# Kernel optimization log

Hardware: AMD Instinct MI355X
Metric: run time of the kernel (lower is better)

The kernel has to match this reference:

```python
import jax, jax.numpy as jnp
import numpy as np

DIM = 512
N_HEADS = 8
HEAD_DIM = DIM // N_HEADS
BN_EPS = 1e-5


def setup_inputs() -> dict:
    key = jax.random.key(0)
    ks = jax.random.split(key, 8)
    B, C, H, W = 16, DIM, 32, 32
    x = jax.random.normal(ks[0], (B, C, H, W), dtype=jnp.float32)
    # 1x1 convs == channel matmuls: stacked q/k/v weights [3, out, in], proj [out, in]
    w_qkv = jax.random.normal(ks[1], (3, DIM, DIM), dtype=jnp.float32) * (DIM ** -0.5)
    w_proj = jax.random.normal(ks[2], (DIM, DIM), dtype=jnp.float32) * (DIM ** -0.5)
    # BatchNorm (inference form) params for q/k/v branches, stacked [3, C]
    bn_gamma = jax.random.uniform(ks[3], (3, DIM), minval=0.5, maxval=1.5)
    bn_beta = jax.random.normal(ks[4], (3, DIM)) * 0.1
    bn_mean = jax.random.normal(ks[5], (3, DIM)) * 0.1
    bn_var = jax.random.uniform(ks[6], (3, DIM), minval=0.5, maxval=1.5)
    return {"x": x, "w_qkv": w_qkv, "w_proj": w_proj, "bn_gamma": bn_gamma,
            "bn_beta": bn_beta, "bn_mean": bn_mean, "bn_var": bn_var}


def _ternary_ste(t):
    # forward: sign(t) in {-1,0,1}; backward: identity (straight-through)
    return t + jax.lax.stop_gradient(jnp.sign(t) - t)


def reference(x, w_qkv, w_proj, bn_gamma, bn_beta, bn_mean, bn_var):
    B, C, H, W = x.shape
    N = H * W
    xf = x.reshape(B, C, N)
    # fused 1x1 conv for q,k,v: [3,B,C,N]
    qkv = jnp.einsum('koc,bcn->kbon', w_qkv, xf)
    # BatchNorm (inference): y = (x - mean)/sqrt(var+eps)*gamma + beta
    s = bn_gamma / jnp.sqrt(bn_var + BN_EPS)          # [3,C]
    b = bn_beta - bn_mean * s                          # [3,C]
    qkv = qkv * s[:, None, :, None] + b[:, None, :, None]
    q = _ternary_ste(qkv[0]).reshape(B, N_HEADS, HEAD_DIM, N)
    k = _ternary_ste(qkv[1]).reshape(B, N_HEADS, HEAD_DIM, N)
    v = qkv[2].reshape(B, N_HEADS, HEAD_DIM, N)
    scale = HEAD_DIM ** -0.5
    attn = jnp.einsum('bhdn,bhen->bhde', q, k) * scale  # [B,h,d,d] channel-wise attn
    attn = jax.nn.softmax(attn, axis=-1)
    out = jnp.einsum('bhde,bhen->bhdn', attn, v).reshape(B, C, N)
    out = jnp.einsum('oc,bcn->bon', w_proj, out) + xf   # proj + residual
    return out.reshape(B, C, H, W)
```

## Files before the change

kernel.cpp:

```cpp
#include <hip/hip_runtime.h>
#include <math.h>

#define BN_EPS 1e-5f

typedef _Float16 f16;
typedef _Float16 f16x4 __attribute__((ext_vector_type(4)));
typedef _Float16 f16x8 __attribute__((ext_vector_type(8)));
typedef float f32x4 __attribute__((ext_vector_type(4)));
typedef int i32x4 __attribute__((ext_vector_type(4)));

static constexpr int BB = 16;
static constexpr int C  = 512;
static constexpr int NP = 1024;
static constexpr int NH = 8;
static constexpr int HD = 64;
static constexpr int M3 = 1536;

static constexpr size_t OFF_WHI = 0;
static constexpr size_t OFF_WLO = 1572864;
static constexpr size_t OFF_WPH = 3145728;
static constexpr size_t OFF_SB  = 3670016;
static constexpr size_t OFF_XTH = 3682304;
static constexpr size_t OFF_XTL = 20459520;
static constexpr size_t OFF_AOT = OFF_XTH;
static constexpr size_t OFF_Q   = 37236736;
static constexpr size_t OFF_K   = 45625344;
static constexpr size_t OFF_VT  = 54013952;

__device__ __forceinline__ void gld16(const void* g, void* l) {
  __builtin_amdgcn_global_load_lds(
      (const __attribute__((address_space(1))) void*)g,
      (__attribute__((address_space(3))) void*)l, 16, 0, 0);
}

__global__ __launch_bounds__(256) void k_convW(
    const float* __restrict__ wqkv, const float* __restrict__ wproj,
    const float* __restrict__ g, const float* __restrict__ be,
    const float* __restrict__ mu, const float* __restrict__ va,
    f16* __restrict__ Whi, f16* __restrict__ Wlo, f16* __restrict__ Wph,
    float* __restrict__ sA, float* __restrict__ bA)
{
  const int i = blockIdx.x * 256 + threadIdx.x;
  if (i < M3 * C) {
    const float w = wqkv[i];
    const f16 h = (f16)w;
    Whi[i] = h;
    Wlo[i] = (f16)(w - (float)h);
  }
  if (i < C * C) Wph[i] = (f16)wproj[i];
  if (i < M3) {
    const float s = g[i] / sqrtf(va[i] + BN_EPS);
    sA[i] = s;
    bA[i] = be[i] - mu[i] * s;
  }
}

__global__ __launch_bounds__(256) void k_convX(
    const float* __restrict__ x, f16* __restrict__ XtH, f16* __restrict__ XtL)
{
  const int k0 = blockIdx.x * 64, n0 = blockIdx.y * 64, b = blockIdx.z;
  __shared__ float ls[64][65];
  const int t = threadIdx.x;
  const float* xp = x + ((size_t)b * C + k0) * NP + n0;
  const int c4 = (t & 15) * 4, r0 = t >> 4;
#pragma unroll
  for (int q = 0; q < 4; ++q) {
    const float4 v = *(const float4*)(xp + (size_t)(r0 + q * 16) * NP + c4);
    ls[r0 + q * 16][c4 + 0] = v.x; ls[r0 + q * 16][c4 + 1] = v.y;
    ls[r0 + q * 16][c4 + 2] = v.z; ls[r0 + q * 16][c4 + 3] = v.w;
  }
  __syncthreads();
  const int n = t >> 2, kk = (t & 3) * 16;
  f16x8 hv0 = {}, hv1 = {}, lv0 = {}, lv1 = {};
#pragma unroll
  for (int q = 0; q < 8; ++q) {
    float v = ls[kk + q][n];
    f16 h = (f16)v;
    hv0[q] = h; lv0[q] = (f16)(v - (float)h);
  }
#pragma unroll
  for (int q = 0; q < 8; ++q) {
    float v = ls[kk + 8 + q][n];
    f16 h = (f16)v;
    hv1[q] = h; lv1[q] = (f16)(v - (float)h);
  }
  const size_t o = ((size_t)b * NP + n0 + n) * C + k0 + kk;
  *(f16x8*)&XtH[o] = hv0; *(f16x8*)&XtH[o + 8] = hv1;
  *(f16x8*)&XtL[o] = lv0; *(f16x8*)&XtL[o + 8] = lv1;
}

__global__ __launch_bounds__(256) void k_qkv_mfma(
    const f16* __restrict__ Whi, const f16* __restrict__ Wlo,
    const f16* __restrict__ XtH, const f16* __restrict__ XtL,
    const float* __restrict__ sA, const float* __restrict__ bA,
    signed char* __restrict__ qw, signed char* __restrict__ kw,
    f16* __restrict__ vt)
{
  __shared__ __align__(16) f16 SMEM[4 * 128 * 32];
  f16* Ah = SMEM;
  f16* Al = SMEM + 4096;
  f16* Bh = SMEM + 8192;
  f16* Bl = SMEM + 12288;

  const int t = threadIdx.x, lane = t & 63, wid = t >> 6;
  const int n0 = blockIdx.x * 128, m0 = blockIdx.y * 128, b = blockIdx.z;

  const f16* A0h = Whi + (size_t)m0 * C;
  const f16* A0l = Wlo + (size_t)m0 * C;
  const f16* B0h = XtH + ((size_t)b * NP + n0) * C;
  const f16* B0l = XtL + ((size_t)b * NP + n0) * C;

  f32x4 acc[4][4];
#pragma unroll
  for (int i = 0; i < 4; ++i)
#pragma unroll
    for (int j = 0; j < 4; ++j) acc[i][j] = (f32x4){0.f, 0.f, 0.f, 0.f};

  const int wm = wid >> 1, wn = wid & 1;
  const int lr = lane & 15, ls = lane >> 4;
  const int srow = wid * 16 + (lane >> 2);
  const int scol = (lane & 3) * 8;

  for (int kc = 0; kc < 512; kc += 32) {
#pragma unroll
    for (int r = 0; r < 2; ++r) {
      const size_t go = (size_t)(r * 64 + srow) * C + kc + scol;
      const int lo = (r * 64 + wid * 16) * 32;
      gld16(A0h + go, &Ah[lo]);
      gld16(A0l + go, &Al[lo]);
      gld16(B0h + go, &Bh[lo]);
      gld16(B0l + go, &Bl[lo]);
    }
    __syncthreads();

    f16x8 ah[4], al[4], bh[4], bl[4];
#pragma unroll
    for (int i = 0; i < 4; ++i) {
      const int ao = (wm * 64 + i * 16 + lr) * 32 + ls * 8;
      ah[i] = *(const f16x8*)&Ah[ao];
      al[i] = *(const f16x8*)&Al[ao];
      const int bo = (wn * 64 + i * 16 + lr) * 32 + ls * 8;
      bh[i] = *(const f16x8*)&Bh[bo];
      bl[i] = *(const f16x8*)&Bl[bo];
    }
#pragma unroll
    for (int i = 0; i < 4; ++i)
#pragma unroll
      for (int j = 0; j < 4; ++j) {
        acc[i][j] = __builtin_amdgcn_mfma_f32_16x16x32_f16(ah[i], bh[j], acc[i][j], 0, 0, 0);
        acc[i][j] = __builtin_amdgcn_mfma_f32_16x16x32_f16(ah[i], bl[j], acc[i][j], 0, 0, 0);
        acc[i][j] = __builtin_amdgcn_mfma_f32_16x16x32_f16(al[i], bh[j], acc[i][j], 0, 0, 0);
      }
    __syncthreads();
  }

  const int kidx = m0 >> 9;
  if (kidx != 2) {
    signed char* dst0 = (kidx == 0) ? qw : kw;
#pragma unroll
    for (int i = 0; i < 4; ++i) {
      float sv[4], bv[4];
#pragma unroll
      for (int r = 0; r < 4; ++r) {
        const int o = m0 + wm * 64 + i * 16 + ls * 4 + r;
        sv[r] = sA[o]; bv[r] = bA[o];
      }
      const int oc0 = (m0 & 511) + wm * 64 + i * 16 + ls * 4;
#pragma unroll
      for (int j = 0; j < 4; ++j) {
        const int n = n0 + wn * 64 + j * 16 + lr;
#pragma unroll
        for (int r = 0; r < 4; ++r) {
          const float y = fmaf(acc[i][j][r], sv[r], bv[r]);
          dst0[((size_t)b * C + oc0 + r) * NP + n] =
              (signed char)((y > 0.f) - (y < 0.f));
        }
      }
    }
  } else {
    const int c0 = m0 & 511;
    for (int hf = 0; hf < 2; ++hf) {
      __syncthreads();
      if (wn == hf) {
#pragma unroll
        for (int i = 0; i < 4; ++i) {
          float sv[4], bv[4];
#pragma unroll
          for (int r = 0; r < 4; ++r) {
            const int o = m0 + wm * 64 + i * 16 + ls * 4 + r;
            sv[r] = sA[o]; bv[r] = bA[o];
          }
#pragma unroll
          for (int j = 0; j < 4; ++j) {
            f16x4 pk;
#pragma unroll
            for (int r = 0; r < 4; ++r)
              pk[r] = (f16)fmaf(acc[i][j][r], sv[r], bv[r]);
            *(f16x4*)&SMEM[(size_t)(j * 16 + lr) * 136 + wm * 64 + i * 16 + ls * 4] = pk;
          }
        }
      }
      __syncthreads();
      const int nl = t >> 2, cc = (t & 3) * 32;
      const f16* src = &SMEM[(size_t)nl * 136 + cc];
      f16x8 r0 = *(const f16x8*)(src + 0);
      f16x8 r1 = *(const f16x8*)(src + 8);
      f16x8 r2 = *(const f16x8*)(src + 16);
      f16x8 r3 = *(const f16x8*)(src + 24);
      f16* dstv = vt + ((size_t)b * NP + n0 + hf * 64 + nl) * C + c0 + cc;
      *(f16x8*)(dstv + 0)  = r0;
      *(f16x8*)(dstv + 8)  = r1;
      *(f16x8*)(dstv + 16) = r2;
      *(f16x8*)(dstv + 24) = r3;
    }
  }
}

__global__ __launch_bounds__(256) void k_attn_fused(
    const signed char* __restrict__ qw, const signed char* __restrict__ kw,
    const f16* __restrict__ vt, f16* __restrict__ aot)
{
  const int half = blockIdx.x;
  const int bh = blockIdx.y;
  const int b = bh >> 3, h = bh & 7;
  const int t = threadIdx.x, lane = t & 63, wid = t >> 6;
  const int dw = wid * 16;
  const int lr = lane & 15, lg = lane >> 4;

  __shared__ f16 ph[64][72];
  __shared__ f16 pl[64][72];
  __shared__ f16 sb[64][72];

  const signed char* qp = qw + ((size_t)b * C + h * HD + dw + lr) * NP;
  const signed char* kp = kw + ((size_t)b * C + h * HD + lr) * NP;

  i32x4 accS[4];
#pragma unroll
  for (int j = 0; j < 4; ++j) accS[j] = (i32x4){0, 0, 0, 0};

#pragma unroll 4
  for (int ks = 0; ks < 16; ++ks) {
    const i32x4 af = *(const i32x4*)(qp + ks * 64 + lg * 16);
#pragma unroll
    for (int j = 0; j < 4; ++j) {
      const i32x4 bf = *(const i32x4*)(kp + (size_t)(j * 16) * NP + ks * 64 + lg * 16);
      accS[j] = __builtin_amdgcn_mfma_i32_16x16x64_i8(af, bf, accS[j], 0, 0, 0);
    }
  }

#pragma unroll
  for (int r = 0; r < 4; ++r) {
    float mx = (float)accS[0][r];
#pragma unroll
    for (int j = 1; j < 4; ++j) mx = fmaxf(mx, (float)accS[j][r]);
    mx = fmaxf(mx, __shfl_xor(mx, 1));
    mx = fmaxf(mx, __shfl_xor(mx, 2));
    mx = fmaxf(mx, __shfl_xor(mx, 4));
    mx = fmaxf(mx, __shfl_xor(mx, 8));
    float pvv[4];
    float sm = 0.f;
#pragma unroll
    for (int j = 0; j < 4; ++j) {
      pvv[j] = expf(((float)accS[j][r] - mx) * 0.125f);
      sm += pvv[j];
    }
    sm += __shfl_xor(sm, 1);
    sm += __shfl_xor(sm, 2);
    sm += __shfl_xor(sm, 4);
    sm += __shfl_xor(sm, 8);
    const float inv = 1.f / sm;
    const int drow = dw + lg * 4 + r;
#pragma unroll
    for (int j = 0; j < 4; ++j) {
      const float p = pvv[j] * inv;
      const f16 hi = (f16)p;
      ph[drow][j * 16 + lr] = hi;
      pl[drow][j * 16 + lr] = (f16)(p - (float)hi);
    }
  }
  __syncthreads();

  const f16x8 pa0h = *(const f16x8*)&ph[dw + lr][lg * 8];
  const f16x8 pa0l = *(const f16x8*)&pl[dw + lr][lg * 8];
  const f16x8 pa1h = *(const f16x8*)&ph[dw + lr][32 + lg * 8];
  const f16x8 pa1l = *(const f16x8*)&pl[dw + lr][32 + lg * 8];

  const f16* vbase = vt + (size_t)b * NP * C + h * HD;
  const int nbase = half * 512;

  for (int nc = 0; nc < 8; ++nc) {
    const int nn0 = nbase + nc * 64;
    __syncthreads();
#pragma unroll
    for (int nt = 0; nt < 4; ++nt) {
      const f16* vp = vbase + (size_t)(nn0 + nt * 16 + lr) * C + lg * 8;
      const f16x8 bv0 = *(const f16x8*)(vp);
      const f16x8 bv1 = *(const f16x8*)(vp + 32);
      f32x4 acc = (f32x4){0.f, 0.f, 0.f, 0.f};
      acc = __builtin_amdgcn_mfma_f32_16x16x32_f16(pa0h, bv0, acc, 0, 0, 0);
      acc = __builtin_amdgcn_mfma_f32_16x16x32_f16(pa0l, bv0, acc, 0, 0, 0);
      acc = __builtin_amdgcn_mfma_f32_16x16x32_f16(pa1h, bv1, acc, 0, 0, 0);
      acc = __builtin_amdgcn_mfma_f32_16x16x32_f16(pa1l, bv1, acc, 0, 0, 0);
      f16x4 pk;
#pragma unroll
      for (int r = 0; r < 4; ++r) pk[r] = (f16)acc[r];
      *(f16x4*)&sb[nt * 16 + lr][dw + lg * 4] = pk;
    }
    __syncthreads();
    const int nl = t >> 2, cc = (t & 3) * 16;
    const f16x8 o0 = *(const f16x8*)&sb[nl][cc];
    const f16x8 o1 = *(const f16x8*)&sb[nl][cc + 8];
    f16* dst = aot + ((size_t)b * NP + nn0 + nl) * C + h * HD + cc;
    *(f16x8*)(dst + 0) = o0;
    *(f16x8*)(dst + 8) = o1;
  }
}

__global__ __launch_bounds__(256) void k_proj_mfma(
    const f16* __restrict__ Wph, const f16* __restrict__ aot,
    const float* __restrict__ X, float* __restrict__ out)
{
  __shared__ __align__(16) f16 Ah[128 * 32];
  __shared__ __align__(16) f16 Bh[128 * 32];

  const int t = threadIdx.x, lane = t & 63, wid = t >> 6;
  const int n0 = blockIdx.x * 128, m0 = blockIdx.y * 128, b = blockIdx.z;

  const f16* A0 = Wph + (size_t)m0 * C;
  const f16* B0 = aot + ((size_t)b * NP + n0) * C;

  f32x4 acc[4][4];
#pragma unroll
  for (int i = 0; i < 4; ++i)
#pragma unroll
    for (int j = 0; j < 4; ++j) acc[i][j] = (f32x4){0.f, 0.f, 0.f, 0.f};

  const int wm = wid >> 1, wn = wid & 1;
  const int lr = lane & 15, ls = lane >> 4;
  const int srow = wid * 16 + (lane >> 2);
  const int scol = (lane & 3) * 8;

  for (int kc = 0; kc < 512; kc += 32) {
#pragma unroll
    for (int r = 0; r < 2; ++r) {
      const size_t go = (size_t)(r * 64 + srow) * C + kc + scol;
      const int lo = (r * 64 + wid * 16) * 32;
      gld16(A0 + go, &Ah[lo]);
      gld16(B0 + go, &Bh[lo]);
    }
    __syncthreads();

    f16x8 ah[4], bh[4];
#pragma unroll
    for (int i = 0; i < 4; ++i) {
      ah[i] = *(const f16x8*)&Ah[(wm * 64 + i * 16 + lr) * 32 + ls * 8];
      bh[i] = *(const f16x8*)&Bh[(wn * 64 + i * 16 + lr) * 32 + ls * 8];
    }
#pragma unroll
    for (int i = 0; i < 4; ++i)
#pragma unroll
      for (int j = 0; j < 4; ++j)
        acc[i][j] = __builtin_amdgcn_mfma_f32_16x16x32_f16(ah[i], bh[j], acc[i][j], 0, 0, 0);
    __syncthreads();
  }

#pragma unroll
  for (int i = 0; i < 4; ++i) {
    const int oc0 = m0 + wm * 64 + i * 16 + ls * 4;
#pragma unroll
    for (int j = 0; j < 4; ++j) {
      const int n = n0 + wn * 64 + j * 16 + lr;
#pragma unroll
      for (int r = 0; r < 4; ++r) {
        const size_t idx = ((size_t)b * C + oc0 + r) * NP + n;
        out[idx] = acc[i][j][r] + X[idx];
      }
    }
  }
}

extern "C" void kernel_launch(void* const* d_in, const int* in_sizes, int n_in,
                              void* d_out, int out_size, void* d_ws, size_t ws_size,
                              hipStream_t stream)
{
  const float* x      = (const float*)d_in[0];
  const float* w_qkv  = (const float*)d_in[1];
  const float* w_proj = (const float*)d_in[2];
  const float* g      = (const float*)d_in[3];
  const float* be     = (const float*)d_in[4];
  const float* mu     = (const float*)d_in[5];
  const float* va     = (const float*)d_in[6];
  float* out = (float*)d_out;

  char* ws = (char*)d_ws;
  f16*  Whi = (f16*)(ws + OFF_WHI);
  f16*  Wlo = (f16*)(ws + OFF_WLO);
  f16*  Wph = (f16*)(ws + OFF_WPH);
  float* sA = (float*)(ws + OFF_SB);
  float* bA = sA + M3;
  f16*  XtH = (f16*)(ws + OFF_XTH);
  f16*  XtL = (f16*)(ws + OFF_XTL);
  f16*  aot = (f16*)(ws + OFF_AOT);
  signed char* qw = (signed char*)(ws + OFF_Q);
  signed char* kw = (signed char*)(ws + OFF_K);
  f16*  vtw = (f16*)(ws + OFF_VT);

  k_convW<<<dim3((M3 * C + 255) / 256), 256, 0, stream>>>(
      w_qkv, w_proj, g, be, mu, va, Whi, Wlo, Wph, sA, bA);
  k_convX<<<dim3(C / 64, NP / 64, BB), 256, 0, stream>>>(x, XtH, XtL);
  k_qkv_mfma<<<dim3(NP / 128, M3 / 128, BB), 256, 0, stream>>>(
      Whi, Wlo, XtH, XtL, sA, bA, qw, kw, vtw);
  k_attn_fused<<<dim3(2, BB * NH), 256, 0, stream>>>(qw, kw, vtw, aot);
  k_proj_mfma<<<dim3(NP / 128, C / 128, BB), 256, 0, stream>>>(Wph, aot, x, out);
}
```

Measured before the change: 152.2 us.

## Use single f16 MFMA for QKV with flagged split-precision sign fixup

Replaces the three-MFMA hi/lo split-precision QKV GEMM with a single f16 MFMA. It computes per-row weight norms and per-pixel input norms so that q/k outputs whose magnitude falls within an error bound of zero can be flagged in a bitmask. A new fixup kernel recomputes only the flagged sign values with hi+lo precision dot products. This cuts the main GEMM's MFMA work and shared-memory traffic by about two thirds, at the cost of extra memsets, atomics, a norm kernel and a sparse fixup pass. The heuristic bound constant, and V now using only the f16 high part, carry accuracy risk.

```diff
diff --git a/kernel.cpp b/kernel.cpp
--- a/kernel.cpp
+++ b/kernel.cpp
@@ -2,6 +2,7 @@
 #include <math.h>
 
 #define BN_EPS 1e-5f
+#define FIXC 3.0e-4f
 
 typedef _Float16 f16;
 typedef _Float16 f16x4 __attribute__((ext_vector_type(4)));
@@ -16,16 +17,19 @@
 static constexpr int HD = 64;
 static constexpr int M3 = 1536;
 
-static constexpr size_t OFF_WHI = 0;
-static constexpr size_t OFF_WLO = 1572864;
-static constexpr size_t OFF_WPH = 3145728;
-static constexpr size_t OFF_SB  = 3670016;
-static constexpr size_t OFF_XTH = 3682304;
-static constexpr size_t OFF_XTL = 20459520;
-static constexpr size_t OFF_AOT = OFF_XTH;
-static constexpr size_t OFF_Q   = 37236736;
-static constexpr size_t OFF_K   = 45625344;
-static constexpr size_t OFF_VT  = 54013952;
+static constexpr size_t OFF_WHI  = 0;
+static constexpr size_t OFF_WLO  = 1572864;
+static constexpr size_t OFF_WPH  = 3145728;
+static constexpr size_t OFF_SB   = 3670016;
+static constexpr size_t OFF_WN   = 3682304;
+static constexpr size_t OFF_XN   = 3686400;
+static constexpr size_t OFF_FLAG = 3751936;
+static constexpr size_t OFF_XTH  = 5849088;
+static constexpr size_t OFF_XTL  = 22626304;
+static constexpr size_t OFF_AOT  = OFF_XTH;
+static constexpr size_t OFF_Q    = 39403520;
+static constexpr size_t OFF_K    = 47792128;
+static constexpr size_t OFF_VT   = 56180736;
 
 __device__ __forceinline__ void gld16(const void* g, void* l) {
   __builtin_amdgcn_global_load_lds(
@@ -55,8 +59,23 @@
   }
 }
 
+__global__ __launch_bounds__(256) void k_wnorm(
+    const float* __restrict__ wqkv, float* __restrict__ wnorm)
+{
+  const int row = blockIdx.x * 4 + (threadIdx.x >> 6);
+  const int lane = threadIdx.x & 63;
+  const float4 v0 = *(const float4*)&wqkv[(size_t)row * C + lane * 8];
+  const float4 v1 = *(const float4*)&wqkv[(size_t)row * C + lane * 8 + 4];
+  float s = v0.x * v0.x + v0.y * v0.y + v0.z * v0.z + v0.w * v0.w
+          + v1.x * v1.x + v1.y * v1.y + v1.z * v1.z + v1.w * v1.w;
+  s += __shfl_xor(s, 1);  s += __shfl_xor(s, 2);  s += __shfl_xor(s, 4);
+  s += __shfl_xor(s, 8);  s += __shfl_xor(s, 16); s += __shfl_xor(s, 32);
+  if (lane == 0) wnorm[row] = sqrtf(s);
+}
+
 __global__ __launch_bounds__(256) void k_convX(
-    const float* __restrict__ x, f16* __restrict__ XtH, f16* __restrict__ XtL)
+    const float* __restrict__ x, f16* __restrict__ XtH, f16* __restrict__ XtL,
+    float* __restrict__ xnorm2)
 {
   const int k0 = blockIdx.x * 64, n0 = blockIdx.y * 64, b = blockIdx.z;
   __shared__ float ls[64][65];
@@ -70,6 +89,12 @@
     ls[r0 + q * 16][c4 + 2] = v.z; ls[r0 + q * 16][c4 + 3] = v.w;
   }
   __syncthreads();
+  if (t < 64) {
+    float s2 = 0.f;
+#pragma unroll
+    for (int q = 0; q < 64; ++q) { const float v = ls[q][t]; s2 = fmaf(v, v, s2); }
+    atomicAdd(&xnorm2[(b << 10) + n0 + t], s2);
+  }
   const int n = t >> 2, kk = (t & 3) * 16;
   f16x8 hv0 = {}, hv1 = {}, lv0 = {}, lv1 = {};
 #pragma unroll
@@ -90,25 +115,21 @@
 }
 
 __global__ __launch_bounds__(256) void k_qkv_mfma(
-    const f16* __restrict__ Whi, const f16* __restrict__ Wlo,
-    const f16* __restrict__ XtH, const f16* __restrict__ XtL,
+    const f16* __restrict__ Whi, const f16* __restrict__ XtH,
     const float* __restrict__ sA, const float* __restrict__ bA,
+    const float* __restrict__ wnorm, const float* __restrict__ xnorm2,
     signed char* __restrict__ qw, signed char* __restrict__ kw,
-    f16* __restrict__ vt)
-{
-  __shared__ __align__(16) f16 SMEM[4 * 128 * 32];
+    f16* __restrict__ vt, unsigned* __restrict__ flagbits)
+{
+  __shared__ __align__(16) f16 SMEM[8704];
   f16* Ah = SMEM;
-  f16* Al = SMEM + 4096;
-  f16* Bh = SMEM + 8192;
-  f16* Bl = SMEM + 12288;
+  f16* Bh = SMEM + 4096;
 
   const int t = threadIdx.x, lane = t & 63, wid = t >> 6;
   const int n0 = blockIdx.x * 128, m0 = blockIdx.y * 128, b = blockIdx.z;
 
   const f16* A0h = Whi + (size_t)m0 * C;
-  const f16* A0l = Wlo + (size_t)m0 * C;
   const f16* B0h = XtH + ((size_t)b * NP + n0) * C;
-  const f16* B0l = XtL + ((size_t)b * NP + n0) * C;
 
   f32x4 acc[4][4];
 #pragma unroll
@@ -127,53 +148,54 @@
       const size_t go = (size_t)(r * 64 + srow) * C + kc + scol;
       const int lo = (r * 64 + wid * 16) * 32;
       gld16(A0h + go, &Ah[lo]);
-      gld16(A0l + go, &Al[lo]);
       gld16(B0h + go, &Bh[lo]);
-      gld16(B0l + go, &Bl[lo]);
-    }
-    __syncthreads();
-
-    f16x8 ah[4], al[4], bh[4], bl[4];
+    }
+    __syncthreads();
+    f16x8 ah[4], bh[4];
 #pragma unroll
     for (int i = 0; i < 4; ++i) {
-      const int ao = (wm * 64 + i * 16 + lr) * 32 + ls * 8;
-      ah[i] = *(const f16x8*)&Ah[ao];
-      al[i] = *(const f16x8*)&Al[ao];
-      const int bo = (wn * 64 + i * 16 + lr) * 32 + ls * 8;
-      bh[i] = *(const f16x8*)&Bh[bo];
-      bl[i] = *(const f16x8*)&Bl[bo];
+      ah[i] = *(const f16x8*)&Ah[(wm * 64 + i * 16 + lr) * 32 + ls * 8];
+      bh[i] = *(const f16x8*)&Bh[(wn * 64 + i * 16 + lr) * 32 + ls * 8];
     }
 #pragma unroll
     for (int i = 0; i < 4; ++i)
 #pragma unroll
-      for (int j = 0; j < 4; ++j) {
+      for (int j = 0; j < 4; ++j)
         acc[i][j] = __builtin_amdgcn_mfma_f32_16x16x32_f16(ah[i], bh[j], acc[i][j], 0, 0, 0);
-        acc[i][j] = __builtin_amdgcn_mfma_f32_16x16x32_f16(ah[i], bl[j], acc[i][j], 0, 0, 0);
-        acc[i][j] = __builtin_amdgcn_mfma_f32_16x16x32_f16(al[i], bh[j], acc[i][j], 0, 0, 0);
-      }
     __syncthreads();
   }
 
   const int kidx = m0 >> 9;
   if (kidx != 2) {
     signed char* dst0 = (kidx == 0) ? qw : kw;
+    float xnrm[4];
+#pragma unroll
+    for (int j = 0; j < 4; ++j)
+      xnrm[j] = sqrtf(xnorm2[(b << 10) + n0 + wn * 64 + j * 16 + lr]);
 #pragma unroll
     for (int i = 0; i < 4; ++i) {
-      float sv[4], bv[4];
+      float sv[4], bv[4], dl[4];
 #pragma unroll
       for (int r = 0; r < 4; ++r) {
         const int o = m0 + wm * 64 + i * 16 + ls * 4 + r;
         sv[r] = sA[o]; bv[r] = bA[o];
+        dl[r] = FIXC * wnorm[o] * sv[r];
       }
       const int oc0 = (m0 & 511) + wm * 64 + i * 16 + ls * 4;
+      const int og0 = m0 + wm * 64 + i * 16 + ls * 4;
 #pragma unroll
       for (int j = 0; j < 4; ++j) {
         const int n = n0 + wn * 64 + j * 16 + lr;
 #pragma unroll
         for (int r = 0; r < 4; ++r) {
-          const float y = fmaf(acc[i][j][r], sv[r], bv[r]);
+          const float z = fmaf(acc[i][j][r], sv[r], bv[r]);
           dst0[((size_t)b * C + oc0 + r) * NP + n] =
-              (signed char)((y > 0.f) - (y < 0.f));
+              (signed char)((z > 0.f) - (z < 0.f));
+          if (fabsf(z) <= dl[r] * xnrm[j]) {
+            const int of = og0 + r;
+            atomicOr(&flagbits[(((size_t)b * NP + n) << 5) + (of >> 5)],
+                     1u << (of & 31));
+          }
         }
       }
     }
@@ -216,6 +238,51 @@
   }
 }
 
+__global__ __launch_bounds__(256) void k_fix(
+    const unsigned* __restrict__ flagbits,
+    const f16* __restrict__ Whi, const f16* __restrict__ Wlo,
+    const f16* __restrict__ XtH, const f16* __restrict__ XtL,
+    const float* __restrict__ sA, const float* __restrict__ bA,
+    signed char* __restrict__ qw, signed char* __restrict__ kw)
+{
+  const int wv = blockIdx.x * 4 + (threadIdx.x >> 6);
+  const int lane = threadIdx.x & 63;
+  const int b = wv >> 10, n = wv & 1023;
+
+  const unsigned* bm = flagbits + ((size_t)wv << 5);
+  const unsigned myw = (lane < 32) ? bm[lane] : 0u;
+  if (__ballot(myw != 0) == 0ULL) return;
+
+  const size_t xo = ((size_t)b * NP + n) * C + lane * 8;
+  const f16x8 bhv = *(const f16x8*)&XtH[xo];
+  const f16x8 blv = *(const f16x8*)&XtL[xo];
+  float xv[8];
+#pragma unroll
+  for (int q = 0; q < 8; ++q) xv[q] = (float)bhv[q] + (float)blv[q];
+
+  for (int w = 0; w < 32; ++w) {
+    unsigned bits = __shfl(myw, w);
+    while (bits) {
+      const int o = w * 32 + __builtin_ctz(bits);
+      bits &= bits - 1;
+      const f16x8 ahv = *(const f16x8*)&Whi[(size_t)o * C + lane * 8];
+      const f16x8 alv = *(const f16x8*)&Wlo[(size_t)o * C + lane * 8];
+      float s = 0.f;
+#pragma unroll
+      for (int q = 0; q < 8; ++q)
+        s = fmaf((float)ahv[q] + (float)alv[q], xv[q], s);
+      s += __shfl_xor(s, 1);  s += __shfl_xor(s, 2);  s += __shfl_xor(s, 4);
+      s += __shfl_xor(s, 8);  s += __shfl_xor(s, 16); s += __shfl_xor(s, 32);
+      if (lane == 0) {
+        const float y = fmaf(s, sA[o], bA[o]);
+        const signed char sg = (signed char)((y > 0.f) - (y < 0.f));
+        if (o < 512) qw[((size_t)b * C + o) * NP + n] = sg;
+        else         kw[((size_t)b * C + (o - 512)) * NP + n] = sg;
+      }
+    }
+  }
+}
+
 __global__ __launch_bounds__(256) void k_attn_fused(
     const signed char* __restrict__ qw, const signed char* __restrict__ kw,
     const f16* __restrict__ vt, f16* __restrict__ aot)
@@ -398,6 +465,9 @@
   f16*  Wph = (f16*)(ws + OFF_WPH);
   float* sA = (float*)(ws + OFF_SB);
   float* bA = sA + M3;
+  float* wn = (float*)(ws + OFF_WN);
+  float* xn2 = (float*)(ws + OFF_XN);
+  unsigned* flagbits = (unsigned*)(ws + OFF_FLAG);
   f16*  XtH = (f16*)(ws + OFF_XTH);
   f16*  XtL = (f16*)(ws + OFF_XTL);
   f16*  aot = (f16*)(ws + OFF_AOT);
@@ -405,11 +475,17 @@
   signed char* kw = (signed char*)(ws + OFF_K);
   f16*  vtw = (f16*)(ws + OFF_VT);
 
+  hipMemsetAsync(xn2, 0, BB * NP * sizeof(float), stream);
+  hipMemsetAsync(flagbits, 0, (size_t)BB * NP * 32 * sizeof(unsigned), stream);
+
   k_convW<<<dim3((M3 * C + 255) / 256), 256, 0, stream>>>(
       w_qkv, w_proj, g, be, mu, va, Whi, Wlo, Wph, sA, bA);
-  k_convX<<<dim3(C / 64, NP / 64, BB), 256, 0, stream>>>(x, XtH, XtL);
+  k_wnorm<<<dim3(256), 256, 0, stream>>>(w_qkv, wn);
+  k_convX<<<dim3(C / 64, NP / 64, BB), 256, 0, stream>>>(x, XtH, XtL, xn2);
   k_qkv_mfma<<<dim3(NP / 128, M3 / 128, BB), 256, 0, stream>>>(
-      Whi, Wlo, XtH, XtL, sA, bA, qw, kw, vtw);
+      Whi, XtH, sA, bA, wn, xn2, qw, kw, vtw, flagbits);
+  k_fix<<<dim3(BB * NP / 4), 256, 0, stream>>>(
+      flagbits, Whi, Wlo, XtH, XtL, sA, bA, qw, kw);
   k_attn_fused<<<dim3(2, BB * NH), 256, 0, stream>>>(qw, kw, vtw, aot);
   k_proj_mfma<<<dim3(NP / 128, C / 128, BB), 256, 0, stream>>>(Wph, aot, x, out);
 }
```

Result: no change. 154.2 us (+1.3%).
